# Optimization experiments

Measured on AMD Instinct MI355X. Metric: run time of the kernel, lower is better.

## Reference

```python
import jax, jax.numpy as jnp
import numpy as np

N_NODES = 100000
N_EDGES = 800000
F_IN = 300
F_PROJ = 256
HIDDEN = 256
F2 = 128
OUT = 4
NEG_SLOPE = 0.2
BN_EPS = 1e-5


def setup_inputs() -> dict:
    key = jax.random.key(0)
    ks = jax.random.split(key, 20)
    def g(k, shape, scale=0.05):
        return jax.random.normal(k, shape, dtype=jnp.float32) * scale
    return {
        "x": jax.random.normal(ks[0], (N_NODES, F_IN), dtype=jnp.float32),
        "edge_index": jax.random.randint(ks[1], (2, N_EDGES), 0, N_NODES),
        "lin_w": g(ks[2], (F_IN, F_PROJ)), "lin_b": jnp.zeros((F_PROJ,), jnp.float32),
        "w1_src": g(ks[3], (F_PROJ, HIDDEN)), "w1_dst": g(ks[4], (F_PROJ, HIDDEN)),
        "a1_src": g(ks[5], (HIDDEN,)), "a1_dst": g(ks[6], (HIDDEN,)),
        "b1": jnp.zeros((HIDDEN,), jnp.float32),
        "w2_src": g(ks[7], (HIDDEN, F2)), "w2_dst": g(ks[8], (HIDDEN, F2)),
        "a2_src": g(ks[9], (F2,)), "a2_dst": g(ks[10], (F2,)),
        "b2": jnp.zeros((F2,), jnp.float32),
        "fc1_w": g(ks[11], (F2, 64)), "fc1_b": jnp.zeros((64,), jnp.float32),
        "bn_g": jnp.ones((64,), jnp.float32), "bn_b": jnp.zeros((64,), jnp.float32),
        "fc2_w": g(ks[12], (64, OUT)), "fc2_b": jnp.zeros((OUT,), jnp.float32),
    }


def gat_conv(x, src, dst, w_src, w_dst, att_src, att_dst, bias, n):
    # PyG GATConv, heads=1: separate src/dst linear, additive attention, LeakyReLU,
    # per-destination segment softmax, weighted scatter-add aggregation.
    h_src = x @ w_src                      # [N, C]
    h_dst = x @ w_dst                      # [N, C]
    a_s = h_src @ att_src                  # [N]
    a_d = h_dst @ att_dst                  # [N]
    e = jax.nn.leaky_relu(a_s[src] + a_d[dst], NEG_SLOPE)  # [E]
    m = jax.ops.segment_max(e, dst, num_segments=n)
    w = jnp.exp(e - m[dst])
    denom = jax.ops.segment_sum(w, dst, num_segments=n)
    alpha = w / (denom[dst] + 1e-16)       # [E]
    out = jax.ops.segment_sum(h_src[src] * alpha[:, None], dst, num_segments=n)
    return out + bias


def reference(x, edge_index, lin_w, lin_b, w1_src, w1_dst, a1_src, a1_dst, b1,
              w2_src, w2_dst, a2_src, a2_dst, b2, fc1_w, fc1_b, bn_g, bn_b,
              fc2_w, fc2_b):
    n = x.shape[0]
    loops = jnp.arange(n)
    src = jnp.concatenate([edge_index[0], loops])  # add_self_loops=True (PyG default)
    dst = jnp.concatenate([edge_index[1], loops])
    h = jax.nn.relu(x @ lin_w + lin_b)             # node-type Linear(-1, 256) + relu
    h = jax.nn.relu(gat_conv(h, src, dst, w1_src, w1_dst, a1_src, a1_dst, b1, n))
    h = jax.nn.relu(gat_conv(h, src, dst, w2_src, w2_dst, a2_src, a2_dst, b2, n))
    h = h @ fc1_w + fc1_b
    mu = jnp.mean(h, axis=0)
    var = jnp.var(h, axis=0)
    h = (h - mu) * jax.lax.rsqrt(var + BN_EPS) * bn_g + bn_b
    h = jax.nn.relu(h)
    h = h @ fc2_w + fc2_b
    return jax.nn.log_softmax(h, axis=-1)
```

## Files before the change

kernel.cpp:

```cpp
#include <hip/hip_runtime.h>
#include <hip/hip_bf16.h>
#include <cmath>

#define NN 100000
#define NE 800000
#define ETOT (NE + NN)
#define MP 100096

#define SCHUNK 512
#define NBLK ((NN + SCHUNK - 1) / SCHUNK)

typedef __attribute__((ext_vector_type(8))) short bf16x8;
typedef __attribute__((ext_vector_type(4))) float f32x4;

__device__ inline void gl_lds16(const void* g, void* l) {
    __builtin_amdgcn_global_load_lds(
        (const __attribute__((address_space(1))) void*)g,
        (__attribute__((address_space(3))) void*)l, 16, 0, 0);
}

__global__ __launch_bounds__(256)
void mfma_gemm(const __hip_bfloat16* __restrict__ Abf,
               const __hip_bfloat16* __restrict__ Btbf,
               const float* __restrict__ bias, void* __restrict__ out,
               const float* __restrict__ dotv, float* __restrict__ dotout,
               int Kp, int ldc, int Mstore, int Nstore, int flags)
{
    __shared__ __align__(16) short As[128 * 32];
    __shared__ __align__(16) short Bs[128 * 32];
    const short* A  = (const short*)Abf;
    const short* Bt = (const short*)Btbf;

    const int tid  = threadIdx.x;
    const int lane = tid & 63;
    const int wv   = tid >> 6;
    const int wr   = (wv >> 1) * 64;
    const int wc   = (wv & 1) * 64;
    const int quad = lane >> 4;
    const int l16  = lane & 15;
    const long bm = (long)blockIdx.x * 128;
    const long bn = (long)blockIdx.y * 128;

    const int r0 = tid >> 2;
    const int c0 = (tid & 3) ^ ((r0 >> 1) & 3);
    const int r1 = r0 + 64;
    const int c1 = (tid & 3) ^ ((r1 >> 1) & 3);
    const short* a_g0 = A + (bm + r0) * (long)Kp + c0 * 8;
    const short* a_g1 = A + (bm + r1) * (long)Kp + c1 * 8;
    const short* b_g0 = Bt + (bn + r0) * (long)Kp + c0 * 8;
    const short* b_g1 = Bt + (bn + r1) * (long)Kp + c1 * 8;
    short* a_l0 = &As[tid * 8];
    short* a_l1 = &As[(tid + 256) * 8];
    short* b_l0 = &Bs[tid * 8];
    short* b_l1 = &Bs[(tid + 256) * 8];

    f32x4 acc[4][4] = {};
    const int xr = (quad ^ ((l16 >> 1) & 3)) * 8;

    for (int k0 = 0; k0 < Kp; k0 += 32) {
        gl_lds16(a_g0 + k0, a_l0);
        gl_lds16(a_g1 + k0, a_l1);
        gl_lds16(b_g0 + k0, b_l0);
        gl_lds16(b_g1 + k0, b_l1);
        __syncthreads();

        bf16x8 af[4], bf[4];
#pragma unroll
        for (int i = 0; i < 4; i++)
            af[i] = *(const bf16x8*)&As[(wr + i * 16 + l16) * 32 + xr];
#pragma unroll
        for (int j = 0; j < 4; j++)
            bf[j] = *(const bf16x8*)&Bs[(wc + j * 16 + l16) * 32 + xr];
#pragma unroll
        for (int i = 0; i < 4; i++)
#pragma unroll
            for (int j = 0; j < 4; j++)
                acc[i][j] = __builtin_amdgcn_mfma_f32_16x16x32_bf16(
                    af[i], bf[j], acc[i][j], 0, 0, 0);
        __syncthreads();
    }

    __hip_bfloat16* outb = (__hip_bfloat16*)out;
    float* outf = (float*)out;
    float dp[16];
#pragma unroll
    for (int t = 0; t < 16; t++) dp[t] = 0.f;

#pragma unroll
    for (int i = 0; i < 4; i++) {
        long row_base = bm + wr + i * 16 + quad * 4;
#pragma unroll
        for (int j = 0; j < 4; j++) {
            long col = bn + wc + j * 16 + l16;
            if (col >= Nstore) continue;
            float bv = bias ? bias[col] : 0.f;
            float dv = dotout ? dotv[col] : 0.f;
#pragma unroll
            for (int r = 0; r < 4; r++) {
                long row = row_base + r;
                float v = acc[i][j][r] + bv;
                if (flags & 1) v = fmaxf(v, 0.f);
                dp[i * 4 + r] = fmaf(v, dv, dp[i * 4 + r]);
                if (row >= Mstore) continue;
                if (flags & 2) outb[row * ldc + col] = __float2bfloat16(v);
                else           outf[row * ldc + col] = v;
            }
        }
    }

    if (dotout) {
#pragma unroll
        for (int t = 0; t < 16; t++) {
            float s = dp[t];
            s += __shfl_xor(s, 1); s += __shfl_xor(s, 2);
            s += __shfl_xor(s, 4); s += __shfl_xor(s, 8);
            if (l16 == 0) {
                long row = bm + wr + (t >> 2) * 16 + quad * 4 + (t & 3);
                if (row < Mstore) atomicAdd(&dotout[row], s);
            }
        }
    }
}

__global__ void cast_x(const float* __restrict__ x, __hip_bfloat16* __restrict__ xb)
{
    int row = blockIdx.x;
    int col = threadIdx.x;
    float v = (row < NN && col < 300) ? x[(size_t)row * 300 + col] : 0.f;
    xb[(size_t)row * 320 + col] = __float2bfloat16(v);
}

__global__ void cast_wT(const float* __restrict__ w, __hip_bfloat16* __restrict__ wt,
                        int K, int N, int Kp, int Np)
{
    int idx = blockIdx.x * 256 + threadIdx.x;
    if (idx >= Np * Kp) return;
    int n = idx / Kp, k = idx % Kp;
    float v = (n < N && k < K) ? w[(size_t)k * N + n] : 0.f;
    wt[idx] = __float2bfloat16(v);
}

__global__ void count_edges(const int* __restrict__ ei, int* __restrict__ counts)
{
    int e = blockIdx.x * blockDim.x + threadIdx.x;
    if (e >= ETOT) return;
    int d = (e < NE) ? ei[NE + e] : (e - NE);
    atomicAdd(&counts[d], 1);
}

__global__ __launch_bounds__(256)
void scan_partial(const int* __restrict__ counts, int* __restrict__ blk)
{
    __shared__ int sh[256];
    const int tid = threadIdx.x;
    const int base = blockIdx.x * SCHUNK + tid * 2;
    int c0 = (base < NN)     ? counts[base]     : 0;
    int c1 = (base + 1 < NN) ? counts[base + 1] : 0;
    sh[tid] = c0 + c1;
    __syncthreads();
    for (int off = 128; off; off >>= 1) {
        if (tid < off) sh[tid] += sh[tid + off];
        __syncthreads();
    }
    if (tid == 0) blk[blockIdx.x] = sh[0];
}

__global__ __launch_bounds__(256)
void scan_blocks(int* __restrict__ blk)
{
    __shared__ int sh[256];
    const int tid = threadIdx.x;
    int v = (tid < NBLK) ? blk[tid] : 0;
    sh[tid] = v;
    __syncthreads();
    for (int off = 1; off < 256; off <<= 1) {
        int u = (tid >= off) ? sh[tid - off] : 0;
        __syncthreads();
        sh[tid] += u;
        __syncthreads();
    }
    if (tid < NBLK) blk[tid] = sh[tid] - v;
}

__global__ __launch_bounds__(256)
void scan_fill(const int* __restrict__ counts, const int* __restrict__ blk,
               int* __restrict__ row_ptr, int* __restrict__ cursor)
{
    __shared__ int sh[256];
    const int tid = threadIdx.x;
    const int i0 = blockIdx.x * SCHUNK + tid * 2;
    int c0 = (i0 < NN)     ? counts[i0]     : 0;
    int c1 = (i0 + 1 < NN) ? counts[i0 + 1] : 0;
    int s = c0 + c1;
    sh[tid] = s;
    __syncthreads();
    for (int off = 1; off < 256; off <<= 1) {
        int u = (tid >= off) ? sh[tid - off] : 0;
        __syncthreads();
        sh[tid] += u;
        __syncthreads();
    }
    int pre = sh[tid] - s + blk[blockIdx.x];
    if (i0 < NN)     { row_ptr[i0] = pre;          cursor[i0] = pre; }
    if (i0 + 1 < NN) { row_ptr[i0 + 1] = pre + c0; cursor[i0 + 1] = pre + c0; }
    if (blockIdx.x == 0 && tid == 0) row_ptr[NN] = ETOT;
}

__global__ void fill_edges(const int* __restrict__ ei, int* __restrict__ cursor,
                           int* __restrict__ csr_src)
{
    int e = blockIdx.x * blockDim.x + threadIdx.x;
    if (e >= ETOT) return;
    int s, d;
    if (e < NE) { s = ei[e]; d = ei[NE + e]; }
    else        { s = e - NE; d = s; }
    int pos = atomicAdd(&cursor[d], 1);
    csr_src[pos] = s;
}

__global__ void wv_kernel(const float* __restrict__ w, const float* __restrict__ a,
                          float* __restrict__ v, int Cin, int Cout)
{
    int i = blockIdx.x * blockDim.x + threadIdx.x;
    if (i >= Cin) return;
    float s = 0.f;
    for (int j = 0; j < Cout; j++) s = fmaf(w[(size_t)i * Cout + j], a[j], s);
    v[i] = s;
}

template<int CPL>
__global__ __launch_bounds__(256)
void gat_agg_wave(const __hip_bfloat16* __restrict__ hsrc,
                  const float* __restrict__ a_s,
                  const float* __restrict__ a_d,
                  const int* __restrict__ row_ptr,
                  const int* __restrict__ csr_src,
                  const float* __restrict__ bias,
                  __hip_bfloat16* __restrict__ outh,
                  const float* __restrict__ dotv,
                  float* __restrict__ dotout)
{
    const int lane = threadIdx.x & 63;
    const int n = blockIdx.x * 4 + (threadIdx.x >> 6);
    if (n >= NN) return;
    const int C = CPL * 64;
    const int start = row_ptr[n];
    const int deg = row_ptr[n + 1] - start;
    const float a_dn = a_d[n];
    const ushort* hp = (const ushort*)hsrc;

    float M = -3e30f, S = 0.f;
    float acc[CPL];
#pragma unroll
    for (int k = 0; k < CPL; k++) acc[k] = 0.f;

    for (int c0 = 0; c0 < deg; c0 += 64) {
        const int cnt = min(64, deg - c0);
        int sj = 0;
        float e = -3e30f;
        if (lane < cnt) {
            sj = csr_src[start + c0 + lane];
            float t = a_s[sj] + a_dn;
            e = (t >= 0.f) ? t : 0.2f * t;
        }
        float cm = e;
#pragma unroll
        for (int off = 32; off; off >>= 1) cm = fmaxf(cm, __shfl_xor(cm, off));
        float newM = fmaxf(M, cm);
        float w = (lane < cnt) ? __expf(e - newM) : 0.f;
        float cs = w;
#pragma unroll
        for (int off = 32; off; off >>= 1) cs += __shfl_xor(cs, off);
        float scale = __expf(M - newM);
        S = S * scale + cs;
#pragma unroll
        for (int k = 0; k < CPL; k++) acc[k] *= scale;
        M = newM;

        for (int j = 0; j < cnt; j++) {
            float wj = __shfl(w, j);
            int s = __shfl(sj, j);
            const ushort* rp = hp + (size_t)s * C + lane * CPL;
            if (CPL == 4) {
                uint2 u = *(const uint2*)rp;
                acc[0] = fmaf(wj, __uint_as_float(u.x << 16), acc[0]);
                acc[1] = fmaf(wj, __uint_as_float(u.x & 0xffff0000u), acc[1]);
                acc[2] = fmaf(wj, __uint_as_float(u.y << 16), acc[2]);
                acc[3] = fmaf(wj, __uint_as_float(u.y & 0xffff0000u), acc[3]);
            } else {
                uint u = *(const uint*)rp;
                acc[0] = fmaf(wj, __uint_as_float(u << 16), acc[0]);
                acc[1] = fmaf(wj, __uint_as_float(u & 0xffff0000u), acc[1]);
            }
        }
    }

    float inv = 1.f / (S + 1e-16f);
    float o[CPL];
    float dp = 0.f;
#pragma unroll
    for (int k = 0; k < CPL; k++) {
        o[k] = fmaxf(acc[k] * inv + bias[lane * CPL + k], 0.f);
        if (dotout) dp = fmaf(o[k], dotv[lane * CPL + k], dp);
    }
    if (CPL == 4) {
        ushort4 pk;
        pk.x = *(ushort*)&(__hip_bfloat16_raw&)(__hip_bfloat16&)(*(__hip_bfloat16[]){__float2bfloat16(o[0])});
        __hip_bfloat16 b0 = __float2bfloat16(o[0]), b1 = __float2bfloat16(o[1]);
        __hip_bfloat16 b2 = __float2bfloat16(o[2]), b3 = __float2bfloat16(o[3]);
        ushort4 v;
        v.x = *(ushort*)&b0; v.y = *(ushort*)&b1; v.z = *(ushort*)&b2; v.w = *(ushort*)&b3;
        *(ushort4*)((ushort*)outh + (size_t)n * C + lane * 4) = v;
    } else {
        __hip_bfloat16 b0 = __float2bfloat16(o[0]), b1 = __float2bfloat16(o[1]);
        ushort2 v;
        v.x = *(ushort*)&b0; v.y = *(ushort*)&b1;
        *(ushort2*)((ushort*)outh + (size_t)n * C + lane * 2) = v;
    }
    if (dotout) {
#pragma unroll
        for (int off = 32; off; off >>= 1) dp += __shfl_xor(dp, off);
        if (lane == 0) dotout[n] = dp;
    }
}

__global__ __launch_bounds__(256)
void bn_stats(const float* __restrict__ h, float* __restrict__ stats)
{
    int col = threadIdx.x & 63;
    int rg = threadIdx.x >> 6;
    int r0 = blockIdx.x * 256;
    int r1 = min(r0 + 256, NN);
    float s = 0.f, s2 = 0.f;
    for (int r = r0 + rg; r < r1; r += 4) {
        float v = h[(size_t)r * 64 + col];
        s += v; s2 += v * v;
    }
    __shared__ float sh[2][4][64];
    sh[0][rg][col] = s; sh[1][rg][col] = s2;
    __syncthreads();
    if (rg == 0) {
        s  = sh[0][0][col] + sh[0][1][col] + sh[0][2][col] + sh[0][3][col];
        s2 = sh[1][0][col] + sh[1][1][col] + sh[1][2][col] + sh[1][3][col];
        atomicAdd(&stats[col], s);
        atomicAdd(&stats[64 + col], s2);
    }
}

__global__ void bn_finalize(const float* __restrict__ stats,
                            const float* __restrict__ g, const float* __restrict__ b,
                            float* __restrict__ ss)
{
    int c = threadIdx.x;
    float mu = stats[c] / (float)NN;
    float var = stats[64 + c] / (float)NN - mu * mu;
    float rs = rsqrtf(var + 1e-5f);
    float sc = rs * g[c];
    ss[c] = sc;
    ss[64 + c] = b[c] - mu * sc;
}

__global__ __launch_bounds__(256)
void final_head(const float* __restrict__ h3, const float* __restrict__ ss,
                const float* __restrict__ fc2_w, const float* __restrict__ fc2_b,
                float* __restrict__ out)
{
    int lane = threadIdx.x & 63;
    int n = blockIdx.x * 4 + (threadIdx.x >> 6);
    if (n >= NN) return;
    float y = h3[(size_t)n * 64 + lane];
    y = fmaxf(y * ss[lane] + ss[64 + lane], 0.f);
    float z[4];
#pragma unroll
    for (int o = 0; o < 4; o++) {
        float p = y * fc2_w[lane * 4 + o];
#pragma unroll
        for (int off = 32; off; off >>= 1) p += __shfl_xor(p, off);
        z[o] = p + fc2_b[o];
    }
    float mx = fmaxf(fmaxf(z[0], z[1]), fmaxf(z[2], z[3]));
    float lse = mx + logf(expf(z[0] - mx) + expf(z[1] - mx) +
                          expf(z[2] - mx) + expf(z[3] - mx));
    if (lane < 4) out[(size_t)n * 4 + lane] = z[lane] - lse;
}

extern "C" void kernel_launch(void* const* d_in, const int* in_sizes, int n_in,
                              void* d_out, int out_size, void* d_ws, size_t ws_size,
                              hipStream_t stream)
{
    const float* x      = (const float*)d_in[0];
    const int*   ei     = (const int*)d_in[1];
    const float* lin_w  = (const float*)d_in[2];
    const float* lin_b  = (const float*)d_in[3];
    const float* w1_src = (const float*)d_in[4];
    const float* w1_dst = (const float*)d_in[5];
    const float* a1_src = (const float*)d_in[6];
    const float* a1_dst = (const float*)d_in[7];
    const float* b1     = (const float*)d_in[8];
    const float* w2_src = (const float*)d_in[9];
    const float* w2_dst = (const float*)d_in[10];
    const float* a2_src = (const float*)d_in[11];
    const float* a2_dst = (const float*)d_in[12];
    const float* b2     = (const float*)d_in[13];
    const float* fc1_w  = (const float*)d_in[14];
    const float* fc1_b  = (const float*)d_in[15];
    const float* bn_g   = (const float*)d_in[16];
    const float* bn_b   = (const float*)d_in[17];
    const float* fc2_w  = (const float*)d_in[18];
    const float* fc2_b  = (const float*)d_in[19];
    float* out = (float*)d_out;

    char* p = (char*)d_ws;
    auto alloc = [&](size_t bytes) { char* r = p; p += (bytes + 255) & ~(size_t)255; return r; };
    char* R1 = alloc((size_t)MP * 320 * 2);
    char* R2 = alloc((size_t)MP * 256 * 2);
    char* R3 = alloc((size_t)MP * 256 * 2);
    __hip_bfloat16* wlinT = (__hip_bfloat16*)alloc(256 * 320 * 2);
    __hip_bfloat16* w1T   = (__hip_bfloat16*)alloc(256 * 256 * 2);
    __hip_bfloat16* w2T   = (__hip_bfloat16*)alloc(128 * 256 * 2);
    __hip_bfloat16* fc1T  = (__hip_bfloat16*)alloc(128 * 128 * 2);
    float* aS1   = (float*)alloc((size_t)NN * 4);
    float* aD1   = (float*)alloc((size_t)NN * 4);
    float* aS2   = (float*)alloc((size_t)NN * 4);
    float* aD2   = (float*)alloc((size_t)NN * 4);
    float* vvec1 = (float*)alloc(256 * 4);
    float* vvec2 = (float*)alloc(256 * 4);
    float* ss    = (float*)alloc(128 * 4);
    float* stats = (float*)alloc(128 * 4);
    int* row_ptr = (int*)alloc((size_t)(NN + 1) * 4);
    int* cursor  = (int*)alloc((size_t)(NN + 1) * 4);
    int* counts  = (int*)alloc((size_t)NN * 4);
    int* blk     = (int*)alloc(256 * 4);
    int* csr_src = (int*)alloc((size_t)ETOT * 4);

    __hip_bfloat16* x_bf  = (__hip_bfloat16*)R1;
    __hip_bfloat16* hsrc1 = (__hip_bfloat16*)R1;
    __hip_bfloat16* h0    = (__hip_bfloat16*)R2;
    __hip_bfloat16* hsrc2 = (__hip_bfloat16*)R2;
    __hip_bfloat16* h2    = (__hip_bfloat16*)(R2 + (size_t)MP * 128 * 2);
    __hip_bfloat16* h1    = (__hip_bfloat16*)R3;
    float*          h3    = (float*)R3;

    const int eb = (ETOT + 255) / 256;
    const int MB = MP / 128;

    hipMemsetAsync(aS1, 0, sizeof(float) * NN * 4, stream);

    hipMemsetAsync(counts, 0, sizeof(int) * NN, stream);
    count_edges<<<eb, 256, 0, stream>>>(ei, counts);
    scan_partial<<<NBLK, 256, 0, stream>>>(counts, blk);
    scan_blocks<<<1, 256, 0, stream>>>(blk);
    scan_fill<<<NBLK, 256, 0, stream>>>(counts, blk, row_ptr, cursor);
    fill_edges<<<eb, 256, 0, stream>>>(ei, cursor, csr_src);

    cast_x<<<MP, 320, 0, stream>>>(x, x_bf);
    cast_wT<<<(256 * 320 + 255) / 256, 256, 0, stream>>>(lin_w, wlinT, 300, 256, 320, 256);
    cast_wT<<<(256 * 256 + 255) / 256, 256, 0, stream>>>(w1_src, w1T, 256, 256, 256, 256);
    cast_wT<<<(128 * 256 + 255) / 256, 256, 0, stream>>>(w2_src, w2T, 256, 128, 256, 128);
    cast_wT<<<(128 * 128 + 255) / 256, 256, 0, stream>>>(fc1_w, fc1T, 128, 64, 128, 128);
    wv_kernel<<<4, 64, 0, stream>>>(w1_dst, a1_dst, vvec1, 256, 256);
    wv_kernel<<<4, 64, 0, stream>>>(w2_dst, a2_dst, vvec2, 256, 128);

    mfma_gemm<<<dim3(MB, 2), 256, 0, stream>>>(x_bf, wlinT, lin_b, h0,
                                               vvec1, aD1, 320, 256, NN, 256, 3);

    mfma_gemm<<<dim3(MB, 2), 256, 0, stream>>>(h0, w1T, nullptr, hsrc1,
                                               a1_src, aS1, 256, 256, NN, 256, 2);
    gat_agg_wave<4><<<(NN + 3) / 4, 256, 0, stream>>>(hsrc1, aS1, aD1, row_ptr,
                                                      csr_src, b1, h1, vvec2, aD2);

    mfma_gemm<<<dim3(MB, 1), 256, 0, stream>>>(h1, w2T, nullptr, hsrc2,
                                               a2_src, aS2, 256, 128, NN, 128, 2);
    gat_agg_wave<2><<<(NN + 3) / 4, 256, 0, stream>>>(hsrc2, aS2, aD2, row_ptr,
                                                      csr_src, b2, h2, nullptr, nullptr);

    mfma_gemm<<<dim3(MB, 1), 256, 0, stream>>>(h2, fc1T, fc1_b, h3,
                                               nullptr, nullptr, 128, 64, NN, 64, 0);
    hipMemsetAsync(stats, 0, sizeof(float) * 128, stream);
    bn_stats<<<(NN + 255) / 256, 256, 0, stream>>>(h3, stats);
    bn_finalize<<<1, 64, 0, stream>>>(stats, bn_g, bn_b, ss);
    final_head<<<(NN + 3) / 4, 256, 0, stream>>>(h3, ss, fc2_w, fc2_b, out);
}
```

Before: 817.7 us.

## Restructure GAT aggregation: per-node lane groups, LDS edge broadcast, 4-way unrolled gathers

Reworks the GAT aggregation kernel so each node is handled by a group of LPN lanes, each lane owning 4 channels. For the 128-channel layer this packs two nodes per wave instead of one. Edge weights and source indices are staged in shared memory instead of broadcast with shuffles, and the gather loop is unrolled four edges at a time so more independent row loads are in flight. This adds LDS traffic and padding work for degree chunks that are not multiples of four, while lowering shuffle overhead and idle lanes. The four attention-score buffers are also merged into one allocation.

```diff
diff --git a/kernel.cpp b/kernel.cpp
--- a/kernel.cpp
+++ b/kernel.cpp
@@ -17,6 +17,11 @@
     __builtin_amdgcn_global_load_lds(
         (const __attribute__((address_space(1))) void*)g,
         (__attribute__((address_space(3))) void*)l, 16, 0, 0);
+}
+
+__device__ inline ushort f2bf(float f) {
+    __hip_bfloat16 b = __float2bfloat16(f);
+    return *(ushort*)&b;
 }
 
 __global__ __launch_bounds__(256)
@@ -228,7 +233,7 @@
     v[i] = s;
 }
 
-template<int CPL>
+template<int LPN>
 __global__ __launch_bounds__(256)
 void gat_agg_wave(const __hip_bfloat16* __restrict__ hsrc,
                   const float* __restrict__ a_s,
@@ -240,87 +245,95 @@
                   const float* __restrict__ dotv,
                   float* __restrict__ dotout)
 {
-    const int lane = threadIdx.x & 63;
-    const int n = blockIdx.x * 4 + (threadIdx.x >> 6);
+    const int C = LPN * 4;
+    const int NPB = 256 / LPN;
+    __shared__ __align__(16) float2 ws_sh[NPB][LPN];
+
+    const int tid  = threadIdx.x;
+    const int slot = tid / LPN;
+    const int sub  = tid % LPN;
+    const int n = blockIdx.x * NPB + slot;
     if (n >= NN) return;
-    const int C = CPL * 64;
+
     const int start = row_ptr[n];
     const int deg = row_ptr[n + 1] - start;
     const float a_dn = a_d[n];
     const ushort* hp = (const ushort*)hsrc;
 
     float M = -3e30f, S = 0.f;
-    float acc[CPL];
-#pragma unroll
-    for (int k = 0; k < CPL; k++) acc[k] = 0.f;
-
-    for (int c0 = 0; c0 < deg; c0 += 64) {
-        const int cnt = min(64, deg - c0);
+    float acc0 = 0.f, acc1 = 0.f, acc2 = 0.f, acc3 = 0.f;
+
+    for (int c0 = 0; c0 < deg; c0 += LPN) {
+        const int cnt = min(LPN, deg - c0);
         int sj = 0;
         float e = -3e30f;
-        if (lane < cnt) {
-            sj = csr_src[start + c0 + lane];
+        if (sub < cnt) {
+            sj = csr_src[start + c0 + sub];
             float t = a_s[sj] + a_dn;
             e = (t >= 0.f) ? t : 0.2f * t;
         }
         float cm = e;
 #pragma unroll
-        for (int off = 32; off; off >>= 1) cm = fmaxf(cm, __shfl_xor(cm, off));
+        for (int off = LPN / 2; off; off >>= 1) cm = fmaxf(cm, __shfl_xor(cm, off));
         float newM = fmaxf(M, cm);
-        float w = (lane < cnt) ? __expf(e - newM) : 0.f;
+        float w = (sub < cnt) ? __expf(e - newM) : 0.f;
         float cs = w;
 #pragma unroll
-        for (int off = 32; off; off >>= 1) cs += __shfl_xor(cs, off);
+        for (int off = LPN / 2; off; off >>= 1) cs += __shfl_xor(cs, off);
         float scale = __expf(M - newM);
         S = S * scale + cs;
-#pragma unroll
-        for (int k = 0; k < CPL; k++) acc[k] *= scale;
+        acc0 *= scale; acc1 *= scale; acc2 *= scale; acc3 *= scale;
         M = newM;
 
-        for (int j = 0; j < cnt; j++) {
-            float wj = __shfl(w, j);
-            int s = __shfl(sj, j);
-            const ushort* rp = hp + (size_t)s * C + lane * CPL;
-            if (CPL == 4) {
-                uint2 u = *(const uint2*)rp;
-                acc[0] = fmaf(wj, __uint_as_float(u.x << 16), acc[0]);
-                acc[1] = fmaf(wj, __uint_as_float(u.x & 0xffff0000u), acc[1]);
-                acc[2] = fmaf(wj, __uint_as_float(u.y << 16), acc[2]);
-                acc[3] = fmaf(wj, __uint_as_float(u.y & 0xffff0000u), acc[3]);
-            } else {
-                uint u = *(const uint*)rp;
-                acc[0] = fmaf(wj, __uint_as_float(u << 16), acc[0]);
-                acc[1] = fmaf(wj, __uint_as_float(u & 0xffff0000u), acc[1]);
-            }
+        ws_sh[slot][sub] = make_float2(w, __int_as_float(sj));
+        const int cnt4 = (cnt + 3) & ~3;
+        const ushort* hpl = hp + sub * 4;
+        for (int j = 0; j < cnt4; j += 4) {
+            float4 p0 = *(const float4*)&ws_sh[slot][j];
+            float4 p1 = *(const float4*)&ws_sh[slot][j + 2];
+            const ushort* r0 = hpl + (size_t)__float_as_int(p0.y) * C;
+            const ushort* r1 = hpl + (size_t)__float_as_int(p0.w) * C;
+            const ushort* r2 = hpl + (size_t)__float_as_int(p1.y) * C;
+            const ushort* r3 = hpl + (size_t)__float_as_int(p1.w) * C;
+            uint2 u0 = *(const uint2*)r0;
+            uint2 u1 = *(const uint2*)r1;
+            uint2 u2 = *(const uint2*)r2;
+            uint2 u3 = *(const uint2*)r3;
+            acc0 = fmaf(p0.x, __uint_as_float(u0.x << 16), acc0);
+            acc1 = fmaf(p0.x, __uint_as_float(u0.x & 0xffff0000u), acc1);
+            acc2 = fmaf(p0.x, __uint_as_float(u0.y << 16), acc2);
+            acc3 = fmaf(p0.x, __uint_as_float(u0.y & 0xffff0000u), acc3);
+            acc0 = fmaf(p0.z, __uint_as_float(u1.x << 16), acc0);
+            acc1 = fmaf(p0.z, __uint_as_float(u1.x & 0xffff0000u), acc1);
+            acc2 = fmaf(p0.z, __uint_as_float(u1.y << 16), acc2);
+            acc3 = fmaf(p0.z, __uint_as_float(u1.y & 0xffff0000u), acc3);
+            acc0 = fmaf(p1.x, __uint_as_float(u2.x << 16), acc0);
+            acc1 = fmaf(p1.x, __uint_as_float(u2.x & 0xffff0000u), acc1);
+            acc2 = fmaf(p1.x, __uint_as_float(u2.y << 16), acc2);
+            acc3 = fmaf(p1.x, __uint_as_float(u2.y & 0xffff0000u), acc3);
+            acc0 = fmaf(p1.z, __uint_as_float(u3.x << 16), acc0);
+            acc1 = fmaf(p1.z, __uint_as_float(u3.x & 0xffff0000u), acc1);
+            acc2 = fmaf(p1.z, __uint_as_float(u3.y << 16), acc2);
+            acc3 = fmaf(p1.z, __uint_as_float(u3.y & 0xffff0000u), acc3);
         }
     }
 
     float inv = 1.f / (S + 1e-16f);
-    float o[CPL];
-    float dp = 0.f;
-#pragma unroll
-    for (int k = 0; k < CPL; k++) {
-        o[k] = fmaxf(acc[k] * inv + bias[lane * CPL + k], 0.f);
-        if (dotout) dp = fmaf(o[k], dotv[lane * CPL + k], dp);
-    }
-    if (CPL == 4) {
-        ushort4 pk;
-        pk.x = *(ushort*)&(__hip_bfloat16_raw&)(__hip_bfloat16&)(*(__hip_bfloat16[]){__float2bfloat16(o[0])});
-        __hip_bfloat16 b0 = __float2bfloat16(o[0]), b1 = __float2bfloat16(o[1]);
-        __hip_bfloat16 b2 = __float2bfloat16(o[2]), b3 = __float2bfloat16(o[3]);
-        ushort4 v;
-        v.x = *(ushort*)&b0; v.y = *(ushort*)&b1; v.z = *(ushort*)&b2; v.w = *(ushort*)&b3;
-        *(ushort4*)((ushort*)outh + (size_t)n * C + lane * 4) = v;
-    } else {
-        __hip_bfloat16 b0 = __float2bfloat16(o[0]), b1 = __float2bfloat16(o[1]);
-        ushort2 v;
-        v.x = *(ushort*)&b0; v.y = *(ushort*)&b1;
-        *(ushort2*)((ushort*)outh + (size_t)n * C + lane * 2) = v;
-    }
+    float o0 = fmaxf(acc0 * inv + bias[sub * 4 + 0], 0.f);
+    float o1 = fmaxf(acc1 * inv + bias[sub * 4 + 1], 0.f);
+    float o2 = fmaxf(acc2 * inv + bias[sub * 4 + 2], 0.f);
+    float o3 = fmaxf(acc3 * inv + bias[sub * 4 + 3], 0.f);
+
+    ushort4 v;
+    v.x = f2bf(o0); v.y = f2bf(o1); v.z = f2bf(o2); v.w = f2bf(o3);
+    *(ushort4*)((ushort*)outh + (size_t)n * C + sub * 4) = v;
+
     if (dotout) {
-#pragma unroll
-        for (int off = 32; off; off >>= 1) dp += __shfl_xor(dp, off);
-        if (lane == 0) dotout[n] = dp;
+        float dp = o0 * dotv[sub * 4 + 0] + o1 * dotv[sub * 4 + 1]
+                 + o2 * dotv[sub * 4 + 2] + o3 * dotv[sub * 4 + 3];
+#pragma unroll
+        for (int off = LPN / 2; off; off >>= 1) dp += __shfl_xor(dp, off);
+        if (sub == 0) dotout[n] = dp;
     }
 }
 
@@ -419,10 +432,11 @@
     __hip_bfloat16* w1T   = (__hip_bfloat16*)alloc(256 * 256 * 2);
     __hip_bfloat16* w2T   = (__hip_bfloat16*)alloc(128 * 256 * 2);
     __hip_bfloat16* fc1T  = (__hip_bfloat16*)alloc(128 * 128 * 2);
-    float* aS1   = (float*)alloc((size_t)NN * 4);
-    float* aD1   = (float*)alloc((size_t)NN * 4);
-    float* aS2   = (float*)alloc((size_t)NN * 4);
-    float* aD2   = (float*)alloc((size_t)NN * 4);
+    float* avec  = (float*)alloc((size_t)NN * 4 * 4);
+    float* aS1 = avec;
+    float* aD1 = avec + NN;
+    float* aS2 = avec + 2 * (size_t)NN;
+    float* aD2 = avec + 3 * (size_t)NN;
     float* vvec1 = (float*)alloc(256 * 4);
     float* vvec2 = (float*)alloc(256 * 4);
     float* ss    = (float*)alloc(128 * 4);
@@ -444,7 +458,7 @@
     const int eb = (ETOT + 255) / 256;
     const int MB = MP / 128;
 
-    hipMemsetAsync(aS1, 0, sizeof(float) * NN * 4, stream);
+    hipMemsetAsync(avec, 0, sizeof(float) * NN * 4, stream);
 
     hipMemsetAsync(counts, 0, sizeof(int) * NN, stream);
     count_edges<<<eb, 256, 0, stream>>>(ei, counts);
@@ -466,13 +480,13 @@
 
     mfma_gemm<<<dim3(MB, 2), 256, 0, stream>>>(h0, w1T, nullptr, hsrc1,
                                                a1_src, aS1, 256, 256, NN, 256, 2);
-    gat_agg_wave<4><<<(NN + 3) / 4, 256, 0, stream>>>(hsrc1, aS1, aD1, row_ptr,
-                                                      csr_src, b1, h1, vvec2, aD2);
+    gat_agg_wave<64><<<(NN + 3) / 4, 256, 0, stream>>>(hsrc1, aS1, aD1, row_ptr,
+                                                       csr_src, b1, h1, vvec2, aD2);
 
     mfma_gemm<<<dim3(MB, 1), 256, 0, stream>>>(h1, w2T, nullptr, hsrc2,
                                                a2_src, aS2, 256, 128, NN, 128, 2);
-    gat_agg_wave<2><<<(NN + 3) / 4, 256, 0, stream>>>(hsrc2, aS2, aD2, row_ptr,
-                                                      csr_src, b2, h2, nullptr, nullptr);
+    gat_agg_wave<32><<<(NN + 7) / 8, 256, 0, stream>>>(hsrc2, aS2, aD2, row_ptr,
+                                                       csr_src, b2, h2, nullptr, nullptr);
 
     mfma_gemm<<<dim3(MB, 1), 256, 0, stream>>>(h2, fc1T, fc1_b, h3,
                                                nullptr, nullptr, 128, 64, NN, 64, 0);
```

Result: faster. 725.0 us (-11.3%).
